# Kernel tuning notes

Hardware: AMD Instinct MI355X
Metric: run time of the kernel (lower is better)

The kernel has to match this reference:

```python
import jax, jax.numpy as jnp
import numpy as np

B, C, REP, H, W = 4, 256, 128, 32, 128
EPS = 1e-5


def _conv1x1(x, w, b=None):
    # x: [B, Cin, H, W], w: [Cout, Cin]
    y = jnp.einsum('oc,bchw->bohw', w, x)
    if b is not None:
        y = y + b[None, :, None, None]
    return y


def _bn_train(x, gamma, beta):
    # BatchNorm2d in training mode: batch stats over (B, H, W)
    mean = jnp.mean(x, axis=(0, 2, 3), keepdims=True)
    var = jnp.var(x, axis=(0, 2, 3), keepdims=True)
    xn = (x - mean) * jax.lax.rsqrt(var + EPS)
    return gamma[None, :, None, None] * xn + beta[None, :, None, None]


def setup_inputs() -> dict:
    key = jax.random.key(0)
    ks = jax.random.split(key, 20)
    f = lambda k, s: jax.random.normal(k, s, dtype=jnp.float32)
    inp = {
        'left': f(ks[0], (B, C, H, W)),
        'right': f(ks[1], (B, C, H, W)),
        'pre_l': jax.random.uniform(ks[2], (B, 1, H, W), dtype=jnp.float32) * W,
        'pre_r': jax.random.uniform(ks[3], (B, 1, H, W), dtype=jnp.float32) * W,
        'query_l': f(ks[4], (B, REP, H, W)),
        'key_l': f(ks[5], (B, REP, H, W)),
        'query_r': f(ks[6], (B, REP, H, W)),
        'key_r': f(ks[7], (B, REP, H, W)),
        # learned 1x1-conv params (kernel stored as [Cout, Cin])
        'theta_w': f(ks[8], (REP, C + 1)) * 0.02,
        'theta_b': f(ks[9], (REP,)) * 0.02,
        'phi_w': f(ks[10], (REP, C)) * 0.02,
        'phi_b': f(ks[11], (REP,)) * 0.02,
        'g_w': f(ks[12], (REP, C)) * 0.02,
        'g_b': f(ks[13], (REP,)) * 0.02,
        'up_w': f(ks[14], (C, REP)) * 0.02,
        'up_b': f(ks[15], (C,)) * 0.02,
        'bn_gamma': f(ks[16], (C,)) * 0.1 + 1.0,
        'bn_beta': f(ks[17], (C,)) * 0.1,
    }
    return inp


def _side(x_q, x_kv, pre, query, key_feat,
          theta_w, theta_b, phi_w, phi_b, g_w, g_b,
          up_w, up_b, bn_gamma, bn_beta):
    hw = H * W
    pre = pre / W
    # theta: [B, hw, REP]
    theta = _conv1x1(jnp.concatenate([x_q, pre], axis=1), theta_w, theta_b)
    theta = theta.reshape(B, REP, hw).transpose(0, 2, 1) + \
        query.reshape(B, REP, hw).transpose(0, 2, 1)
    # phi: [B, REP, hw]
    phi = _conv1x1(x_kv, phi_w, phi_b).reshape(B, REP, hw) + \
        key_feat.reshape(B, REP, hw)
    # g: [B, hw, REP]
    g = _conv1x1(x_kv, g_w, g_b).reshape(B, REP, hw).transpose(0, 2, 1)
    # attention over all hw key positions: [B, hw, hw]
    atten = jax.nn.softmax(jnp.einsum('bqc,bck->bqk', theta, phi), axis=-1)
    # soft-argmax over key column index (arange(W) tiled H times along key axis)
    col_idx = jnp.tile(jnp.arange(W, dtype=jnp.float32), H)  # [hw]
    exp_col = jnp.einsum('bqk,k->bq', atten, col_idx)        # [B, hw]
    q_col = (jnp.arange(hw, dtype=jnp.float32) % W)[None, :]  # [1, hw]
    index = (q_col - exp_col).reshape(B, H, W)
    # value aggregation + residual projection
    after = jnp.einsum('bqk,bkc->bqc', atten, g)
    after = after.transpose(0, 2, 1).reshape(B, REP, H, W)
    out = x_q + _bn_train(_conv1x1(after, up_w, up_b), bn_gamma, bn_beta)
    return out, index


def reference(left, right, pre_l, pre_r, query_l, key_l, query_r, key_r,
              theta_w, theta_b, phi_w, phi_b, g_w, g_b,
              up_w, up_b, bn_gamma, bn_beta):
    l_n, index_l = _side(left, right, pre_l, query_l, key_r,
                         theta_w, theta_b, phi_w, phi_b, g_w, g_b,
                         up_w, up_b, bn_gamma, bn_beta)
    r_n, index_r = _side(right, left, pre_r, query_r, key_l,
                         theta_w, theta_b, phi_w, phi_b, g_w, g_b,
                         up_w, up_b, bn_gamma, bn_beta)
    return (l_n, r_n, index_l, index_r)
```

## Files before the change

### kernel.cpp

```cpp
#include <hip/hip_runtime.h>


typedef unsigned short u16;
typedef unsigned int   u32;
typedef float        floatx4 __attribute__((ext_vector_type(4)));
typedef unsigned int uintx4  __attribute__((ext_vector_type(4)));
typedef unsigned int uintx2  __attribute__((ext_vector_type(2)));
typedef _Float16     half8   __attribute__((ext_vector_type(8)));
typedef __fp16       fp16x2  __attribute__((ext_vector_type(2)));

#define HW 4096
#define CB 256
#define RP 128
#define EPSF 1e-5f

static __device__ __forceinline__ u16 f2bf(float f) {
  u32 u = __float_as_uint(f);
  u32 r = u + 0x7FFFu + ((u >> 16) & 1u);
  return (u16)(r >> 16);
}
static __device__ __forceinline__ float bf2f(u16 h) {
  return __uint_as_float(((u32)h) << 16);
}
static __device__ __forceinline__ u16 f2h(float f) {
  _Float16 h = (_Float16)f;
  return __builtin_bit_cast(u16, h);
}
static __device__ __forceinline__ float h2f(u16 h) {
  return (float)__builtin_bit_cast(_Float16, h);
}
static __device__ __forceinline__ half8 as_h8(uintx4 v) {
  return __builtin_bit_cast(half8, v);
}
static __device__ __forceinline__ u32 pkrtz(float a, float b) {
  fp16x2 h = __builtin_amdgcn_cvt_pkrtz(a, b);
  return __builtin_bit_cast(u32, h);
}
static __device__ __forceinline__ u32 pk2h(float a, float b) {
  return (u32)f2h(a) | ((u32)f2h(b) << 16);
}
static __device__ __forceinline__ void barrier_nodrain() {
  __builtin_amdgcn_sched_barrier(0);
  asm volatile("s_waitcnt lgkmcnt(0)" ::: "memory");
  __builtin_amdgcn_s_barrier();
  __builtin_amdgcn_sched_barrier(0);
}

union Pk4 { u16 u[4]; uintx2 v; };

struct ProjCfg {
  const float* x; const float* w; const float* bias;
  const float* add; const float* pre; u16* out;
  int wstride; int transposed;
};
struct ProjCfg6 { ProjCfg c[6]; };

#define XSTR 40

__global__ __launch_bounds__(256) void ra_projm(ProjCfg6 cfg)
{
  __shared__ u16 x_lds[128 * XSTR];
  __shared__ u16 w_lds[128 * XSTR];
  const ProjCfg C = cfg.c[blockIdx.x >> 7];
  const int inner = blockIdx.x & 127;
  const int b    = inner >> 5;
  const int pos0 = (inner & 31) * 128;
  const int tid  = threadIdx.x;
  const int wv   = tid >> 6;
  const int lane = tid & 63;
  const int ln16 = lane & 15;
  const int quad = lane >> 4;
  const int mbase = wv * 32;

  const int xc0 = (tid & 7) * 4, xp0 = (tid >> 3) * 4;
  const int wrr = tid >> 1, wch = (tid & 1) * 16;

  floatx4 acc[2][8];
  #pragma unroll
  for (int mt = 0; mt < 2; mt++)
    #pragma unroll
    for (int nt = 0; nt < 8; nt++) acc[mt][nt] = (floatx4)0.0f;

  #pragma unroll 1
  for (int cc = 0; cc < 8; ++cc) {
    floatx4 xr[4];
    #pragma unroll
    for (int i = 0; i < 4; i++)
      xr[i] = *(const floatx4*)(C.x + (size_t)(b * CB + cc * 32 + xc0 + i) * HW + pos0 + xp0);
    float ww[16];
    {
      const float* wp = C.w + (size_t)wrr * C.wstride + cc * 32 + wch;
      #pragma unroll
      for (int i = 0; i < 16; i++) ww[i] = wp[i];
    }
    __syncthreads();
    #pragma unroll
    for (int pp = 0; pp < 4; pp++) {
      uintx2 v;
      v[0] = pk2h(xr[0][pp], xr[1][pp]);
      v[1] = pk2h(xr[2][pp], xr[3][pp]);
      *(uintx2*)&x_lds[(xp0 + pp) * XSTR + xc0] = v;
    }
    {
      uintx4 v0, v1;
      v0[0] = pk2h(ww[0], ww[1]);  v0[1] = pk2h(ww[2], ww[3]);
      v0[2] = pk2h(ww[4], ww[5]);  v0[3] = pk2h(ww[6], ww[7]);
      v1[0] = pk2h(ww[8], ww[9]);  v1[1] = pk2h(ww[10], ww[11]);
      v1[2] = pk2h(ww[12], ww[13]); v1[3] = pk2h(ww[14], ww[15]);
      *(uintx4*)&w_lds[wrr * XSTR + wch]     = v0;
      *(uintx4*)&w_lds[wrr * XSTR + wch + 8] = v1;
    }
    __syncthreads();
    if (!C.transposed) {
      half8 a0 = as_h8(*(const uintx4*)&w_lds[(mbase + ln16) * XSTR + quad * 8]);
      half8 a1 = as_h8(*(const uintx4*)&w_lds[(mbase + 16 + ln16) * XSTR + quad * 8]);
      #pragma unroll
      for (int nt = 0; nt < 8; nt++) {
        half8 bf = as_h8(*(const uintx4*)&x_lds[(nt * 16 + ln16) * XSTR + quad * 8]);
        acc[0][nt] = __builtin_amdgcn_mfma_f32_16x16x32_f16(a0, bf, acc[0][nt], 0, 0, 0);
        acc[1][nt] = __builtin_amdgcn_mfma_f32_16x16x32_f16(a1, bf, acc[1][nt], 0, 0, 0);
      }
    } else {
      half8 a0 = as_h8(*(const uintx4*)&x_lds[(mbase + ln16) * XSTR + quad * 8]);
      half8 a1 = as_h8(*(const uintx4*)&x_lds[(mbase + 16 + ln16) * XSTR + quad * 8]);
      #pragma unroll
      for (int nt = 0; nt < 8; nt++) {
        half8 bf = as_h8(*(const uintx4*)&w_lds[(nt * 16 + ln16) * XSTR + quad * 8]);
        acc[0][nt] = __builtin_amdgcn_mfma_f32_16x16x32_f16(a0, bf, acc[0][nt], 0, 0, 0);
        acc[1][nt] = __builtin_amdgcn_mfma_f32_16x16x32_f16(a1, bf, acc[1][nt], 0, 0, 0);
      }
    }
  }

  if (!C.transposed) {
    #pragma unroll
    for (int mt = 0; mt < 2; mt++) {
      const int r0 = mbase + mt * 16 + quad * 4;
      floatx4 bi = *(const floatx4*)(C.bias + r0);
      float wc[4];
      if (C.pre) {
        #pragma unroll
        for (int rr = 0; rr < 4; rr++) wc[rr] = C.w[(size_t)(r0 + rr) * C.wstride + 256];
      }
      #pragma unroll
      for (int nt = 0; nt < 8; nt++) {
        const int pos = pos0 + nt * 16 + ln16;
        floatx4 v = acc[mt][nt];
        #pragma unroll
        for (int rr = 0; rr < 4; rr++) v[rr] += bi[rr];
        if (C.pre) {
          const float pv = C.pre[(size_t)b * HW + pos] * (1.f / 128.f);
          #pragma unroll
          for (int rr = 0; rr < 4; rr++) v[rr] += pv * wc[rr];
        }
        if (C.add) {
          #pragma unroll
          for (int rr = 0; rr < 4; rr++)
            v[rr] += C.add[(size_t)(b * RP + r0 + rr) * HW + pos];
        }
        Pk4 pk;
        #pragma unroll
        for (int rr = 0; rr < 4; rr++) pk.u[rr] = f2h(v[rr]);
        *(uintx2*)(C.out + (size_t)(b * HW + pos) * RP + r0) = pk.v;
      }
    }
  } else {
    #pragma unroll
    for (int nt = 0; nt < 8; nt++) {
      const int r = nt * 16 + ln16;
      const float bs = C.bias[r];
      #pragma unroll
      for (int mt = 0; mt < 2; mt++) {
        const int pv = pos0 + mbase + mt * 16 + quad * 4;
        floatx4 v = acc[mt][nt];
        Pk4 pk;
        #pragma unroll
        for (int rr = 0; rr < 4; rr++) pk.u[rr] = f2h(v[rr] + bs);
        *(uintx2*)(C.out + (size_t)(b * RP + r) * HW + pv) = pk.v;
      }
    }
  }
}

__global__ __launch_bounds__(256) void ra_flash(
    const u16* __restrict__ thetaL, const u16* __restrict__ phiTL,
    const u16* __restrict__ gTL,
    const u16* __restrict__ thetaR, const u16* __restrict__ phiTR,
    const u16* __restrict__ gTR,
    u16* __restrict__ pO, float* __restrict__ mla)
{
  __shared__ uintx4 phi_lds[16 * 65];
  __shared__ uintx4 g_lds[8 * 129];
  __shared__ u16 P_lds[4][16 * 76];

  const int tid  = threadIdx.x;
  const int bx   = blockIdx.x;
  const int side = bx >> 9;
  const int sbx  = bx & 511;
  const u16* __restrict__ theta = side ? thetaR : thetaL;
  const u16* __restrict__ phiT  = side ? phiTR  : phiTL;
  const u16* __restrict__ gT    = side ? gTR    : gTL;

  const int b    = sbx >> 7;
  const int rem  = sbx & 127;
  const int q0   = (rem >> 1) * 64;
  const int split= rem & 1;
  const int kbase= split * 2048;
  const int wv   = tid >> 6;
  const int lane = tid & 63;
  const int ln16 = lane & 15;
  const int quad = lane >> 4;

  uintx4 aq[4];
  {
    const uintx4* tr = (const uintx4*)(theta + (size_t)(b * HW + q0 + wv * 16 + ln16) * RP);
    #pragma unroll
    for (int c = 0; c < 4; c++) aq[c] = tr[c * 4 + quad];
  }

  floatx4 accO[8];
  #pragma unroll
  for (int v = 0; v < 8; v++) accO[v] = (floatx4)0.0f;
  float m_q = -3.0e38f, l_q = 0.f, aC_q = 0.f;

  const int sk  = tid >> 4, scb = tid & 15;
  const int gv_ = tid >> 3, gcb = tid & 7;

  uintx4 sp[4], sg[4];
  #pragma unroll
  for (int i = 0; i < 4; i++) {
    sp[i] = *(const uintx4*)(phiT + (size_t)(b * HW + kbase + i * 16 + sk) * RP + scb * 8);
    sg[i] = *(const uintx4*)(gT + (size_t)(b * RP + i * 32 + gv_) * HW + kbase + gcb * 8);
  }

  #pragma unroll 1
  for (int j = 0; j < 32; j++) {
    #pragma unroll
    for (int i = 0; i < 4; i++) {
      phi_lds[scb * 65 + i * 16 + sk] = sp[i];
      g_lds[gcb * 129 + i * 32 + gv_] = sg[i];
    }
    if (j < 31) {
      const int k0n = kbase + (j + 1) * 64;
      #pragma unroll
      for (int i = 0; i < 4; i++) {
        sp[i] = *(const uintx4*)(phiT + (size_t)(b * HW + k0n + i * 16 + sk) * RP + scb * 8);
        sg[i] = *(const uintx4*)(gT + (size_t)(b * RP + i * 32 + gv_) * HW + k0n + gcb * 8);
      }
    }
    barrier_nodrain();

    floatx4 sf[4];
    #pragma unroll
    for (int s = 0; s < 4; s++) sf[s] = (floatx4)0.0f;
    __builtin_amdgcn_s_setprio(1);
    #pragma unroll
    for (int c = 0; c < 4; c++) {
      half8 bth = as_h8(aq[c]);
      #pragma unroll
      for (int s = 0; s < 4; s++) {
        uintx4 ap = phi_lds[(c * 4 + quad) * 65 + s * 16 + ln16];
        sf[s] = __builtin_amdgcn_mfma_f32_16x16x32_f16(as_h8(ap), bth, sf[s], 0, 0, 0);
      }
    }
    __builtin_amdgcn_s_setprio(0);

    float ms0 = fmaxf(fmaxf(sf[0][0], sf[0][1]), fmaxf(sf[0][2], sf[0][3]));
    float ms1 = fmaxf(fmaxf(sf[1][0], sf[1][1]), fmaxf(sf[1][2], sf[1][3]));
    float ms2 = fmaxf(fmaxf(sf[2][0], sf[2][1]), fmaxf(sf[2][2], sf[2][3]));
    float ms3 = fmaxf(fmaxf(sf[3][0], sf[3][1]), fmaxf(sf[3][2], sf[3][3]));
    float mx = fmaxf(fmaxf(ms0, ms1), fmaxf(ms2, ms3));
    mx = fmaxf(mx, __shfl_xor(mx, 16));
    mx = fmaxf(mx, __shfl_xor(mx, 32));
    if (__any(mx > m_q + 8.f)) {
      const float mnew  = fmaxf(m_q, mx);
      const float alpha = __expf(m_q - mnew);
      m_q = mnew;
      l_q *= alpha; aC_q *= alpha;
      #pragma unroll
      for (int v = 0; v < 8; v++) accO[v] *= alpha;
    }
    const float colbase = (float)((j * 64) & 127) + (float)(quad * 4);
    float ps = 0.f, pc = 0.f;
    #pragma unroll
    for (int s = 0; s < 4; s++) {
      float p0 = __expf(sf[s][0] - m_q);
      float p1 = __expf(sf[s][1] - m_q);
      float p2 = __expf(sf[s][2] - m_q);
      float p3 = __expf(sf[s][3] - m_q);
      ps += (p0 + p1) + (p2 + p3);
      const float cb = colbase + (float)(s * 16);
      pc += p0 * cb + p1 * (cb + 1.f) + p2 * (cb + 2.f) + p3 * (cb + 3.f);
      uintx2 pkv;
      pkv[0] = pkrtz(p0, p1);
      pkv[1] = pkrtz(p2, p3);
      *(uintx2*)&P_lds[wv][ln16 * 76 + s * 16 + quad * 4] = pkv;
    }
    ps += __shfl_xor(ps, 16); ps += __shfl_xor(ps, 32);
    pc += __shfl_xor(pc, 16); pc += __shfl_xor(pc, 32);
    l_q  += ps;
    aC_q += pc;

    half8 pb0 = as_h8(*(const uintx4*)&P_lds[wv][ln16 * 76 + quad * 8]);
    half8 pb1 = as_h8(*(const uintx4*)&P_lds[wv][ln16 * 76 + 32 + quad * 8]);
    __builtin_amdgcn_s_setprio(1);
    #pragma unroll
    for (int vt = 0; vt < 8; vt++) {
      uintx4 ag0 = g_lds[quad * 129 + vt * 16 + ln16];
      uintx4 ag1 = g_lds[(4 + quad) * 129 + vt * 16 + ln16];
      accO[vt] = __builtin_amdgcn_mfma_f32_16x16x32_f16(as_h8(ag0), pb0, accO[vt], 0, 0, 0);
      accO[vt] = __builtin_amdgcn_mfma_f32_16x16x32_f16(as_h8(ag1), pb1, accO[vt], 0, 0, 0);
    }
    __builtin_amdgcn_s_setprio(0);
    barrier_nodrain();
  }

  const int q = q0 + wv * 16 + ln16;
  const size_t p = (size_t)side * 32768 + (size_t)split * 16384 + b * HW + q;
  u16* orow = pO + p * RP;
  const float invl = 1.f / l_q;
  #pragma unroll
  for (int vt = 0; vt < 8; vt++) {
    uintx2 pkv;
    pkv[0] = pkrtz(accO[vt][0] * invl, accO[vt][1] * invl);
    pkv[1] = pkrtz(accO[vt][2] * invl, accO[vt][3] * invl);
    *(uintx2*)(orow + vt * 16 + quad * 4) = pkv;
  }
  if (quad == 0) {
    floatx4 m4; m4[0] = m_q; m4[1] = l_q; m4[2] = aC_q; m4[3] = 0.f;
    *(floatx4*)(mla + p * 4) = m4;
  }
}

__global__ __launch_bounds__(256) void ra_combine(
    const u16* __restrict__ pO, const float* __restrict__ mla,
    u16* __restrict__ afterL, u16* __restrict__ afterR,
    float* __restrict__ idxL, float* __restrict__ idxR)
{
  const int t = threadIdx.x;
  const int pp = blockIdx.x * 2 + (t >> 7);
  const int side = pp >> 14;
  const int p = pp & 16383;
  const int v = t & 127;
  const size_t base = (size_t)side * 32768;
  const floatx4 A  = *(const floatx4*)(mla + (base + p) * 4);
  const floatx4 Bv = *(const floatx4*)(mla + (base + 16384 + p) * 4);
  const float M  = fmaxf(A[0], Bv[0]);
  const float w0 = __expf(A[0] - M), w1 = __expf(Bv[0] - M);
  const float s0 = w0 * A[1], s1 = w1 * Bv[1];
  const float inv = 1.0f / (s0 + s1);
  const float a0 = h2f(pO[(base + p) * RP + v]);
  const float a1 = h2f(pO[(base + 16384 + p) * RP + v]);
  u16* after = side ? afterR : afterL;
  after[(size_t)p * RP + v] = f2h((s0 * a0 + s1 * a1) * inv);
  if (v == 0) {
    float* idx = side ? idxR : idxL;
    idx[p] = (float)(p & 127) - (w0 * A[2] + w1 * Bv[2]) * inv;
  }
}

#define WSTR 136

__global__ __launch_bounds__(256) void ra_upm(
    const u16* __restrict__ afterL, const u16* __restrict__ afterR,
    const float* __restrict__ w, const float* __restrict__ bias,
    u16* __restrict__ yL, u16* __restrict__ yR)
{
  __shared__ u16 w_lds[128 * WSTR];
  const int tid  = threadIdx.x;
  const int bx   = blockIdx.x;
  const int side = bx >> 8;
  const int sbx  = bx & 255;
  const u16* __restrict__ after = side ? afterR : afterL;
  u16* __restrict__ y = side ? yR : yL;
  const int b    = sbx >> 6;
  const int pos0 = ((sbx >> 1) & 31) * 128;
  const int hc   = sbx & 1;
  const int wv   = tid >> 6;
  const int lane = tid & 63;
  const int ln16 = lane & 15;
  const int quad = lane >> 4;

  {
    const int co = tid >> 1, rh = (tid & 1) * 64;
    const float* wp = w + (size_t)(hc * 128 + co) * RP + rh;
    #pragma unroll
    for (int i = 0; i < 8; i++) {
      floatx4 f0 = *(const floatx4*)(wp + i * 8);
      floatx4 f1 = *(const floatx4*)(wp + i * 8 + 4);
      uintx4 v;
      v[0] = pk2h(f0[0], f0[1]); v[1] = pk2h(f0[2], f0[3]);
      v[2] = pk2h(f1[0], f1[1]); v[3] = pk2h(f1[2], f1[3]);
      *(uintx4*)&w_lds[co * WSTR + rh + i * 8] = v;
    }
  }
  __syncthreads();

  floatx4 acc[2][8];
  #pragma unroll
  for (int mt = 0; mt < 2; mt++)
    #pragma unroll
    for (int nt = 0; nt < 8; nt++) acc[mt][nt] = (floatx4)0.0f;

  #pragma unroll
  for (int kk = 0; kk < 4; kk++) {
    half8 a[2];
    #pragma unroll
    for (int mt = 0; mt < 2; mt++)
      a[mt] = as_h8(*(const uintx4*)(after +
          (size_t)(b * HW + pos0 + wv * 32 + mt * 16 + ln16) * RP + kk * 32 + quad * 8));
    #pragma unroll
    for (int nt = 0; nt < 8; nt++) {
      half8 bf = as_h8(*(const uintx4*)&w_lds[(nt * 16 + ln16) * WSTR + kk * 32 + quad * 8]);
      acc[0][nt] = __builtin_amdgcn_mfma_f32_16x16x32_f16(a[0], bf, acc[0][nt], 0, 0, 0);
      acc[1][nt] = __builtin_amdgcn_mfma_f32_16x16x32_f16(a[1], bf, acc[1][nt], 0, 0, 0);
    }
  }

  #pragma unroll
  for (int nt = 0; nt < 8; nt++) {
    const int co = hc * 128 + nt * 16 + ln16;
    const float bs = bias[co];
    #pragma unroll
    for (int mt = 0; mt < 2; mt++) {
      const int pv = pos0 + wv * 32 + mt * 16 + quad * 4;
      floatx4 v = acc[mt][nt];
      Pk4 pk;
      #pragma unroll
      for (int rr = 0; rr < 4; rr++) pk.u[rr] = f2bf(v[rr] + bs);
      *(uintx2*)(y + (size_t)(b * CB + co) * HW + pv) = pk.v;
    }
  }
}

__global__ __launch_bounds__(256) void ra_stats(
    const u16* __restrict__ yL, const u16* __restrict__ yR,
    float* __restrict__ stL, float* __restrict__ stR)
{
  const int side = blockIdx.x >> 8;
  const int c = blockIdx.x & 255;
  const u16* __restrict__ y = side ? yR : yL;
  float* __restrict__ stats = side ? stR : stL;
  const int tid = threadIdx.x;
  float s = 0.f, sq = 0.f;
  for (int b = 0; b < 4; b++) {
    const uintx4* row = (const uintx4*)(y + (size_t)(b * CB + c) * HW);
    #pragma unroll
    for (int t = 0; t < 2; t++) {
      uintx4 rv = row[tid + t * 256];
      #pragma unroll
      for (int k = 0; k < 4; k++) {
        float a0 = bf2f((u16)(rv[k] & 0xffffu));
        float a1 = bf2f((u16)(rv[k] >> 16));
        s += a0 + a1; sq += a0 * a0 + a1 * a1;
      }
    }
  }
  #pragma unroll
  for (int m = 1; m < 64; m <<= 1) { s += __shfl_xor(s, m); sq += __shfl_xor(sq, m); }
  __shared__ float red[8];
  const int wv = tid >> 6;
  if ((tid & 63) == 0) { red[wv * 2] = s; red[wv * 2 + 1] = sq; }
  __syncthreads();
  if (tid == 0) {
    s  = red[0] + red[2] + red[4] + red[6];
    sq = red[1] + red[3] + red[5] + red[7];
    const float mean = s * (1.f / 16384.f);
    const float var  = sq * (1.f / 16384.f) - mean * mean;
    stats[2 * c]     = mean;
    stats[2 * c + 1] = rsqrtf(var + EPSF);
  }
}

__global__ __launch_bounds__(256) void ra_fin(
    const float* __restrict__ left, const float* __restrict__ right,
    const u16* __restrict__ yL, const u16* __restrict__ yR,
    const float* __restrict__ stL, const float* __restrict__ stR,
    const float* __restrict__ gamma, const float* __restrict__ beta,
    float* __restrict__ out)
{
  const size_t e = (size_t)blockIdx.x * 256 + threadIdx.x;
  const int side = (int)(e >> 20);
  const size_t e4 = e & 1048575;
  const int c = (int)((e4 >> 10) & 255);
  const float* x = side ? right : left;
  const u16* y = side ? yR : yL;
  const float* stats = side ? stR : stL;
  const float mean = stats[2 * c], rstd = stats[2 * c + 1];
  const float ga = gamma[c], be = beta[c];
  floatx4 xv = ((const floatx4*)x)[e4];
  uintx2 yv = ((const uintx2*)y)[e4];
  float f0 = bf2f((u16)(yv[0] & 0xffffu));
  float f1 = bf2f((u16)(yv[0] >> 16));
  float f2 = bf2f((u16)(yv[1] & 0xffffu));
  float f3 = bf2f((u16)(yv[1] >> 16));
  floatx4 o;
  o[0] = xv[0] + ga * ((f0 - mean) * rstd) + be;
  o[1] = xv[1] + ga * ((f1 - mean) * rstd) + be;
  o[2] = xv[2] + ga * ((f2 - mean) * rstd) + be;
  o[3] = xv[3] + ga * ((f3 - mean) * rstd) + be;
  ((floatx4*)out)[(size_t)side * 1048576 + e4] = o;
}

extern "C" void kernel_launch(void* const* d_in, const int* in_sizes, int n_in,
                              void* d_out, int out_size, void* d_ws, size_t ws_size,
                              hipStream_t stream)
{
  const float* left    = (const float*)d_in[0];
  const float* right   = (const float*)d_in[1];
  const float* pre_l   = (const float*)d_in[2];
  const float* pre_r   = (const float*)d_in[3];
  const float* query_l = (const float*)d_in[4];
  const float* key_l   = (const float*)d_in[5];
  const float* query_r = (const float*)d_in[6];
  const float* key_r   = (const float*)d_in[7];
  const float* theta_w = (const float*)d_in[8];
  const float* theta_b = (const float*)d_in[9];
  const float* phi_w   = (const float*)d_in[10];
  const float* phi_b   = (const float*)d_in[11];
  const float* g_w     = (const float*)d_in[12];
  const float* g_b     = (const float*)d_in[13];
  const float* up_w    = (const float*)d_in[14];
  const float* up_b    = (const float*)d_in[15];
  const float* bn_g    = (const float*)d_in[16];
  const float* bn_b    = (const float*)d_in[17];
  float* out = (float*)d_out;

  char* ws = (char*)d_ws;
  const size_t SZ = (size_t)4 * HW * RP * 2;
  u16* thetaL = (u16*)(ws);
  u16* phiTL  = (u16*)(ws + 1 * SZ);
  u16* gTL    = (u16*)(ws + 2 * SZ);
  u16* thetaR = (u16*)(ws + 3 * SZ);
  u16* phiTR  = (u16*)(ws + 4 * SZ);
  u16* gTR    = (u16*)(ws + 5 * SZ);
  u16* afterL = (u16*)(ws + 6 * SZ);
  u16* afterR = (u16*)(ws + 7 * SZ);
  u16* pO     = (u16*)(ws + 8 * SZ);
  u16* yL     = (u16*)(ws + 8 * SZ);
  u16* yR     = (u16*)(ws + 10 * SZ);
  float* stL  = (float*)(ws + 12 * SZ);
  float* stR  = (float*)(ws + 12 * SZ + 2048);
  float* mla  = (float*)(ws + 12 * SZ + 8192);

  dim3 blk(256);
  ProjCfg6 pc;
  pc.c[0] = { left,  theta_w, theta_b, query_l, pre_l,   thetaL, 257, 0 };
  pc.c[1] = { right, phi_w,   phi_b,   key_r,   nullptr, phiTL,  256, 0 };
  pc.c[2] = { right, g_w,     g_b,     nullptr, nullptr, gTL,    256, 1 };
  pc.c[3] = { right, theta_w, theta_b, query_r, pre_r,   thetaR, 257, 0 };
  pc.c[4] = { left,  phi_w,   phi_b,   key_l,   nullptr, phiTR,  256, 0 };
  pc.c[5] = { left,  g_w,     g_b,     nullptr, nullptr, gTR,    256, 1 };
  ra_projm<<<768, blk, 0, stream>>>(pc);

  ra_flash<<<1024, blk, 0, stream>>>(thetaL, phiTL, gTL, thetaR, phiTR, gTR, pO, mla);
  ra_combine<<<16384, blk, 0, stream>>>(pO, mla, afterL, afterR,
                                        out + 8388608, out + 8404992);
  ra_upm<<<512, blk, 0, stream>>>(afterL, afterR, up_w, up_b, yL, yR);
  ra_stats<<<512, blk, 0, stream>>>(yL, yR, stL, stR);
  ra_fin<<<8192, blk, 0, stream>>>(left, right, yL, yR, stL, stR, bn_g, bn_b, out);

  (void)in_sizes; (void)n_in; (void)out_size; (void)ws_size;
}
```

Baseline: 337.7 us.

## Drop split-K in flash attention, fuse combine, compute row sums via MFMA

Each flash block now processes all keys for its query tile instead of half, which removes the separate combine kernel and the partial-output and max/sum buffers. The softmax denominator and the column-weighted sum for the soft-argmax are accumulated with extra MFMAs against a constant coefficient matrix, using alternating accumulators to keep fp16 column indices small. This saves a launch and intermediate global traffic, but halves the grid size and doubles per-block loop length, which may reduce parallelism.

```diff
diff --git a/kernel.cpp b/kernel.cpp
--- a/kernel.cpp
+++ b/kernel.cpp
@@ -187,7 +187,8 @@
     const u16* __restrict__ gTL,
     const u16* __restrict__ thetaR, const u16* __restrict__ phiTR,
     const u16* __restrict__ gTR,
-    u16* __restrict__ pO, float* __restrict__ mla)
+    u16* __restrict__ afterL, u16* __restrict__ afterR,
+    float* __restrict__ idxL, float* __restrict__ idxR)
 {
   __shared__ uintx4 phi_lds[16 * 65];
   __shared__ uintx4 g_lds[8 * 129];
@@ -195,17 +196,14 @@
 
   const int tid  = threadIdx.x;
   const int bx   = blockIdx.x;
-  const int side = bx >> 9;
-  const int sbx  = bx & 511;
+  const int side = bx >> 8;
+  const int sbx  = bx & 255;
   const u16* __restrict__ theta = side ? thetaR : thetaL;
   const u16* __restrict__ phiT  = side ? phiTR  : phiTL;
   const u16* __restrict__ gT    = side ? gTR    : gTL;
 
-  const int b    = sbx >> 7;
-  const int rem  = sbx & 127;
-  const int q0   = (rem >> 1) * 64;
-  const int split= rem & 1;
-  const int kbase= split * 2048;
+  const int b    = sbx >> 6;
+  const int q0   = (sbx & 63) * 64;
   const int wv   = tid >> 6;
   const int lane = tid & 63;
   const int ln16 = lane & 15;
@@ -218,10 +216,23 @@
     for (int c = 0; c < 4; c++) aq[c] = tr[c * 4 + quad];
   }
 
+  half8 cf0, cf1;
+  {
+    #pragma unroll
+    for (int i = 0; i < 8; i++) {
+      float c0 = (ln16 == 0) ? (float)(quad * 8 + i)      : (ln16 == 1 ? 1.f : 0.f);
+      float c1 = (ln16 == 0) ? (float)(32 + quad * 8 + i) : (ln16 == 1 ? 1.f : 0.f);
+      cf0[i] = (_Float16)c0;
+      cf1[i] = (_Float16)c1;
+    }
+  }
+
   floatx4 accO[8];
   #pragma unroll
   for (int v = 0; v < 8; v++) accO[v] = (floatx4)0.0f;
-  float m_q = -3.0e38f, l_q = 0.f, aC_q = 0.f;
+  floatx4 accE  = (floatx4)0.0f;
+  floatx4 accEo = (floatx4)0.0f;
+  float m_q = -3.0e38f;
 
   const int sk  = tid >> 4, scb = tid & 15;
   const int gv_ = tid >> 3, gcb = tid & 7;
@@ -229,19 +240,19 @@
   uintx4 sp[4], sg[4];
   #pragma unroll
   for (int i = 0; i < 4; i++) {
-    sp[i] = *(const uintx4*)(phiT + (size_t)(b * HW + kbase + i * 16 + sk) * RP + scb * 8);
-    sg[i] = *(const uintx4*)(gT + (size_t)(b * RP + i * 32 + gv_) * HW + kbase + gcb * 8);
+    sp[i] = *(const uintx4*)(phiT + (size_t)(b * HW + i * 16 + sk) * RP + scb * 8);
+    sg[i] = *(const uintx4*)(gT + (size_t)(b * RP + i * 32 + gv_) * HW + gcb * 8);
   }
 
   #pragma unroll 1
-  for (int j = 0; j < 32; j++) {
+  for (int j = 0; j < 64; j++) {
     #pragma unroll
     for (int i = 0; i < 4; i++) {
       phi_lds[scb * 65 + i * 16 + sk] = sp[i];
       g_lds[gcb * 129 + i * 32 + gv_] = sg[i];
     }
-    if (j < 31) {
-      const int k0n = kbase + (j + 1) * 64;
+    if (j < 63) {
+      const int k0n = (j + 1) * 64;
       #pragma unroll
       for (int i = 0; i < 4; i++) {
         sp[i] = *(const uintx4*)(phiT + (size_t)(b * HW + k0n + i * 16 + sk) * RP + scb * 8);
@@ -276,30 +287,21 @@
       const float mnew  = fmaxf(m_q, mx);
       const float alpha = __expf(m_q - mnew);
       m_q = mnew;
-      l_q *= alpha; aC_q *= alpha;
+      accE *= alpha; accEo *= alpha;
       #pragma unroll
       for (int v = 0; v < 8; v++) accO[v] *= alpha;
     }
-    const float colbase = (float)((j * 64) & 127) + (float)(quad * 4);
-    float ps = 0.f, pc = 0.f;
     #pragma unroll
     for (int s = 0; s < 4; s++) {
       float p0 = __expf(sf[s][0] - m_q);
       float p1 = __expf(sf[s][1] - m_q);
       float p2 = __expf(sf[s][2] - m_q);
       float p3 = __expf(sf[s][3] - m_q);
-      ps += (p0 + p1) + (p2 + p3);
-      const float cb = colbase + (float)(s * 16);
-      pc += p0 * cb + p1 * (cb + 1.f) + p2 * (cb + 2.f) + p3 * (cb + 3.f);
       uintx2 pkv;
       pkv[0] = pkrtz(p0, p1);
       pkv[1] = pkrtz(p2, p3);
       *(uintx2*)&P_lds[wv][ln16 * 76 + s * 16 + quad * 4] = pkv;
     }
-    ps += __shfl_xor(ps, 16); ps += __shfl_xor(ps, 32);
-    pc += __shfl_xor(pc, 16); pc += __shfl_xor(pc, 32);
-    l_q  += ps;
-    aC_q += pc;
 
     half8 pb0 = as_h8(*(const uintx4*)&P_lds[wv][ln16 * 76 + quad * 8]);
     half8 pb1 = as_h8(*(const uintx4*)&P_lds[wv][ln16 * 76 + 32 + quad * 8]);
@@ -311,14 +313,27 @@
       accO[vt] = __builtin_amdgcn_mfma_f32_16x16x32_f16(as_h8(ag0), pb0, accO[vt], 0, 0, 0);
       accO[vt] = __builtin_amdgcn_mfma_f32_16x16x32_f16(as_h8(ag1), pb1, accO[vt], 0, 0, 0);
     }
+    if (j & 1) {
+      accEo = __builtin_amdgcn_mfma_f32_16x16x32_f16(cf0, pb0, accEo, 0, 0, 0);
+      accEo = __builtin_amdgcn_mfma_f32_16x16x32_f16(cf1, pb1, accEo, 0, 0, 0);
+    } else {
+      accE  = __builtin_amdgcn_mfma_f32_16x16x32_f16(cf0, pb0, accE, 0, 0, 0);
+      accE  = __builtin_amdgcn_mfma_f32_16x16x32_f16(cf1, pb1, accE, 0, 0, 0);
+    }
     __builtin_amdgcn_s_setprio(0);
     barrier_nodrain();
   }
 
+  const float l0 = accE[1] + accEo[1];
+  const float a0 = accE[0] + accEo[0] + 64.f * accEo[1];
+  const float l_all  = __shfl(l0, ln16);
+  const float aC_all = __shfl(a0, ln16);
+
   const int q = q0 + wv * 16 + ln16;
-  const size_t p = (size_t)side * 32768 + (size_t)split * 16384 + b * HW + q;
-  u16* orow = pO + p * RP;
-  const float invl = 1.f / l_q;
+  const size_t p = (size_t)b * HW + q;
+  u16* after = side ? afterR : afterL;
+  u16* orow = after + p * RP;
+  const float invl = 1.f / l_all;
   #pragma unroll
   for (int vt = 0; vt < 8; vt++) {
     uintx2 pkv;
@@ -327,35 +342,8 @@
     *(uintx2*)(orow + vt * 16 + quad * 4) = pkv;
   }
   if (quad == 0) {
-    floatx4 m4; m4[0] = m_q; m4[1] = l_q; m4[2] = aC_q; m4[3] = 0.f;
-    *(floatx4*)(mla + p * 4) = m4;
-  }
-}
-
-__global__ __launch_bounds__(256) void ra_combine(
-    const u16* __restrict__ pO, const float* __restrict__ mla,
-    u16* __restrict__ afterL, u16* __restrict__ afterR,
-    float* __restrict__ idxL, float* __restrict__ idxR)
-{
-  const int t = threadIdx.x;
-  const int pp = blockIdx.x * 2 + (t >> 7);
-  const int side = pp >> 14;
-  const int p = pp & 16383;
-  const int v = t & 127;
-  const size_t base = (size_t)side * 32768;
-  const floatx4 A  = *(const floatx4*)(mla + (base + p) * 4);
-  const floatx4 Bv = *(const floatx4*)(mla + (base + 16384 + p) * 4);
-  const float M  = fmaxf(A[0], Bv[0]);
-  const float w0 = __expf(A[0] - M), w1 = __expf(Bv[0] - M);
-  const float s0 = w0 * A[1], s1 = w1 * Bv[1];
-  const float inv = 1.0f / (s0 + s1);
-  const float a0 = h2f(pO[(base + p) * RP + v]);
-  const float a1 = h2f(pO[(base + 16384 + p) * RP + v]);
-  u16* after = side ? afterR : afterL;
-  after[(size_t)p * RP + v] = f2h((s0 * a0 + s1 * a1) * inv);
-  if (v == 0) {
     float* idx = side ? idxR : idxL;
-    idx[p] = (float)(p & 127) - (w0 * A[2] + w1 * Bv[2]) * inv;
+    idx[p] = (float)(q & 127) - aC_all * invl;
   }
 }
 
@@ -536,12 +524,10 @@
   u16* gTR    = (u16*)(ws + 5 * SZ);
   u16* afterL = (u16*)(ws + 6 * SZ);
   u16* afterR = (u16*)(ws + 7 * SZ);
-  u16* pO     = (u16*)(ws + 8 * SZ);
   u16* yL     = (u16*)(ws + 8 * SZ);
   u16* yR     = (u16*)(ws + 10 * SZ);
   float* stL  = (float*)(ws + 12 * SZ);
   float* stR  = (float*)(ws + 12 * SZ + 2048);
-  float* mla  = (float*)(ws + 12 * SZ + 8192);
 
   dim3 blk(256);
   ProjCfg6 pc;
@@ -553,9 +539,9 @@
   pc.c[5] = { left,  g_w,     g_b,     nullptr, nullptr, gTR,    256, 1 };
   ra_projm<<<768, blk, 0, stream>>>(pc);
 
-  ra_flash<<<1024, blk, 0, stream>>>(thetaL, phiTL, gTL, thetaR, phiTR, gTR, pO, mla);
-  ra_combine<<<16384, blk, 0, stream>>>(pO, mla, afterL, afterR,
-                                        out + 8388608, out + 8404992);
+  ra_flash<<<512, blk, 0, stream>>>(thetaL, phiTL, gTL, thetaR, phiTR, gTR,
+                                    afterL, afterR,
+                                    out + 8388608, out + 8404992);
   ra_upm<<<512, blk, 0, stream>>>(afterL, afterR, up_w, up_b, yL, yR);
   ra_stats<<<512, blk, 0, stream>>>(yL, yR, stL, stR);
   ra_fin<<<8192, blk, 0, stream>>>(left, right, yL, yR, stL, stR, bn_g, bn_b, out);
```

After: 318.2 us. 1.06x faster.
